# Optimization experiments

Hardware: AMD Instinct MI355X
Metric: run time of the kernel (lower is better)

Reference implementation:

```python
import jax, jax.numpy as jnp
import numpy as np
import math

EMBED_DIM = 1024
NUM_HEADS = 16
HEAD_DIM = EMBED_DIM // NUM_HEADS
MAX_POS = 512
SPARSE_TOPK = 32
B, T = 8, 512


def setup_inputs() -> dict:
    key = jax.random.key(0)
    ks = jax.random.split(key, 12)
    s = 1.0 / math.sqrt(EMBED_DIM)
    inp = {
        "x": jax.random.normal(ks[0], (B, T, EMBED_DIM), dtype=jnp.float32),
        "Wq": jax.random.uniform(ks[1], (EMBED_DIM, EMBED_DIM), jnp.float32, -s, s),
        "bq": jax.random.uniform(ks[2], (EMBED_DIM,), jnp.float32, -s, s),
        "Wk": jax.random.uniform(ks[3], (EMBED_DIM, EMBED_DIM), jnp.float32, -s, s),
        "bk": jax.random.uniform(ks[4], (EMBED_DIM,), jnp.float32, -s, s),
        "Wv": jax.random.uniform(ks[5], (EMBED_DIM, EMBED_DIM), jnp.float32, -s, s),
        "bv": jax.random.uniform(ks[6], (EMBED_DIM,), jnp.float32, -s, s),
        "Wo": jax.random.uniform(ks[7], (EMBED_DIM, EMBED_DIM), jnp.float32, -s, s),
        "bo": jax.random.uniform(ks[8], (EMBED_DIM,), jnp.float32, -s, s),
        "head_gates": jnp.ones((NUM_HEADS,), dtype=jnp.float32),
        "rel_bias": 0.02 * jax.random.normal(ks[9], (2 * MAX_POS - 1, NUM_HEADS), dtype=jnp.float32),
    }
    return inp


def reference(x, Wq, bq, Wk, bk, Wv, bv, Wo, bo, head_gates, rel_bias):
    Bb, Tt, C = x.shape
    H, D = NUM_HEADS, HEAD_DIM
    # projections -> [B, H, T, D]
    q = (x @ Wq.T + bq).reshape(Bb, Tt, H, D).transpose(0, 2, 1, 3)
    k = (x @ Wk.T + bk).reshape(Bb, Tt, H, D).transpose(0, 2, 1, 3)
    v = (x @ Wv.T + bv).reshape(Bb, Tt, H, D).transpose(0, 2, 1, 3)
    scores = jnp.einsum("bhqd,bhkd->bhqk", q, k) / math.sqrt(D)
    # gathered relative-position bias: rel[i,j] = j - i + MAX_POS - 1
    idx = jnp.arange(Tt)
    rel = idx[None, :] - idx[:, None] + (MAX_POS - 1)          # [T, T]
    pos_bias = rel_bias[rel].transpose(2, 0, 1)[None]          # [1, H, T, T]
    scores = scores + pos_bias
    if SPARSE_TOPK > 0:
        # keep only top-k entries per row; threshold == k-th largest value,
        # equivalent to torch.topk + scatter into a full -inf matrix
        topk_vals, _ = jax.lax.top_k(scores, SPARSE_TOPK)
        thresh = topk_vals[..., -1:]
        scores = jnp.where(scores >= thresh, scores, -jnp.inf)
    weights = jax.nn.softmax(scores, axis=-1)                  # dropout is identity (p=0, eval)
    gated = weights * head_gates[None, :, None, None]
    attn_out = jnp.einsum("bhqk,bhkd->bhqd", gated, v)
    attn_out = attn_out.transpose(0, 2, 1, 3).reshape(Bb, Tt, C)
    return attn_out @ Wo.T + bo
```

## Files before the change

### kernel.cpp

```cpp
#include <hip/hip_runtime.h>
#include <math.h>

#define EMBED 1024
#define NHEAD 16
#define HDIM  64
#define MAXPOS 512
#define TOPK  32
#define BB    8
#define TTT   512
#define BT    (BB*TTT)

__global__ __launch_bounds__(256, 2)
void gemm_qk_f64(const float* __restrict__ A,
                 const float* __restrict__ Wq, const float* __restrict__ bq_,
                 const float* __restrict__ Wk, const float* __restrict__ bk_,
                 float* __restrict__ outq, float* __restrict__ outk)
{
    __shared__ float As[16][132];
    __shared__ float Bs[16][68];
    const int t  = threadIdx.x;
    const int mb = blockIdx.x;
    const int yy = blockIdx.y;
    const int nb = yy & 15;
    const float* __restrict__ W    = (yy < 16) ? Wq  : Wk;
    const float* __restrict__ bias = (yy < 16) ? bq_ : bk_;
    float*                    out  = (yy < 16) ? outq : outk;
    const int tr = t >> 4, tc = t & 15;

    double acc[8][4] = {};

    for (int kt = 0; kt < 1024; kt += 16) {
        #pragma unroll
        for (int i = 0; i < 2; i++) {
            int L   = t + i * 256;
            int row = L >> 2;
            int cg  = (L & 3) * 4;
            float4 a4 = *(const float4*)&A[(size_t)(mb*128 + row)*1024 + kt + cg];
            As[cg+0][row] = a4.x; As[cg+1][row] = a4.y;
            As[cg+2][row] = a4.z; As[cg+3][row] = a4.w;
        }
        {
            int row = t >> 2, cg = (t & 3) * 4;
            float4 b4 = *(const float4*)&W[(size_t)(nb*64 + row)*1024 + kt + cg];
            Bs[cg+0][row] = b4.x; Bs[cg+1][row] = b4.y;
            Bs[cg+2][row] = b4.z; Bs[cg+3][row] = b4.w;
        }
        __syncthreads();
        #pragma unroll
        for (int kk = 0; kk < 16; kk++) {
            float a[8], bv[4];
            *(float4*)&a[0]  = *(const float4*)&As[kk][tr*8];
            *(float4*)&a[4]  = *(const float4*)&As[kk][tr*8+4];
            *(float4*)&bv[0] = *(const float4*)&Bs[kk][tc*4];
            double bd[4] = {(double)bv[0], (double)bv[1], (double)bv[2], (double)bv[3]};
            #pragma unroll
            for (int i = 0; i < 8; i++) {
                double ad = (double)a[i];
                #pragma unroll
                for (int j = 0; j < 4; j++)
                    acc[i][j] = fma(ad, bd[j], acc[i][j]);
            }
        }
        __syncthreads();
    }

    #pragma unroll
    for (int i = 0; i < 8; i++) {
        int token = mb*128 + tr*8 + i;
        int b  = token >> 9, tt = token & 511;
        int c0 = nb*64 + tc*4;
        float4 v;
        v.x = (float)(acc[i][0] + (double)bias[c0+0]);
        v.y = (float)(acc[i][1] + (double)bias[c0+1]);
        v.z = (float)(acc[i][2] + (double)bias[c0+2]);
        v.w = (float)(acc[i][3] + (double)bias[c0+3]);
        *(float4*)&out[(((size_t)b*NHEAD + nb)*TTT + tt)*HDIM + tc*4] = v;
    }
}

__global__ __launch_bounds__(256, 2)
void gemm_nt(const float* __restrict__ A, const float* __restrict__ W,
             const float* __restrict__ bias, float* __restrict__ out,
             int scatter)
{
    __shared__ float As[16][132];
    __shared__ float Bs[16][132];
    const int t  = threadIdx.x;
    const int mb = blockIdx.x;
    const int nb = blockIdx.y;
    const int tr = t >> 4, tc = t & 15;

    float acc[8][8] = {};

    for (int kt = 0; kt < 1024; kt += 16) {
        #pragma unroll
        for (int i = 0; i < 2; i++) {
            int L   = t + i * 256;
            int row = L >> 2;
            int cg  = (L & 3) * 4;
            float4 a4 = *(const float4*)&A[(size_t)(mb*128 + row)*1024 + kt + cg];
            As[cg+0][row] = a4.x; As[cg+1][row] = a4.y;
            As[cg+2][row] = a4.z; As[cg+3][row] = a4.w;
            float4 b4 = *(const float4*)&W[(size_t)(nb*128 + row)*1024 + kt + cg];
            Bs[cg+0][row] = b4.x; Bs[cg+1][row] = b4.y;
            Bs[cg+2][row] = b4.z; Bs[cg+3][row] = b4.w;
        }
        __syncthreads();
        #pragma unroll
        for (int kk = 0; kk < 16; kk++) {
            float a[8], bv[8];
            *(float4*)&a[0]  = *(const float4*)&As[kk][tr*8];
            *(float4*)&a[4]  = *(const float4*)&As[kk][tr*8+4];
            *(float4*)&bv[0] = *(const float4*)&Bs[kk][tc*8];
            *(float4*)&bv[4] = *(const float4*)&Bs[kk][tc*8+4];
            #pragma unroll
            for (int i = 0; i < 8; i++)
                #pragma unroll
                for (int j = 0; j < 8; j++)
                    acc[i][j] = fmaf(a[i], bv[j], acc[i][j]);
        }
        __syncthreads();
    }

    if (scatter) {
        #pragma unroll
        for (int i = 0; i < 8; i++) {
            int token = mb*128 + tr*8 + i;
            int b  = token >> 9, tt = token & 511;
            #pragma unroll
            for (int jg = 0; jg < 2; jg++) {
                int c = nb*128 + tc*8 + jg*4;
                int h = c >> 6, d = c & 63;
                float4 v;
                v.x = acc[i][jg*4+0] + bias[c+0];
                v.y = acc[i][jg*4+1] + bias[c+1];
                v.z = acc[i][jg*4+2] + bias[c+2];
                v.w = acc[i][jg*4+3] + bias[c+3];
                *(float4*)&out[(((size_t)b*NHEAD + h)*TTT + tt)*HDIM + d] = v;
            }
        }
    } else {
        #pragma unroll
        for (int i = 0; i < 8; i++) {
            int token = mb*128 + tr*8 + i;
            #pragma unroll
            for (int jg = 0; jg < 2; jg++) {
                int c = nb*128 + tc*8 + jg*4;
                float4 v;
                v.x = acc[i][jg*4+0] + bias[c+0];
                v.y = acc[i][jg*4+1] + bias[c+1];
                v.z = acc[i][jg*4+2] + bias[c+2];
                v.w = acc[i][jg*4+3] + bias[c+3];
                *(float4*)&out[(size_t)token*1024 + c] = v;
            }
        }
    }
}

__global__ __launch_bounds__(512, 4)
void attn_kernel(const float* __restrict__ qb, const float* __restrict__ kb,
                 const float* __restrict__ vb, const float* __restrict__ gates,
                 const float* __restrict__ relb, float* __restrict__ aout)
{
    __shared__ float qs[32][68];
    __shared__ union {
        float ks[128][68];
        struct { float w[32][64]; unsigned short c[32][64]; } sp;
    } u;

    const int t    = threadIdx.x;
    const int lane = t & 63, wv = t >> 6;
    const int qt   = blockIdx.x;
    const int bh   = blockIdx.y;
    const int h    = bh & 15, b = bh >> 4;
    const int qrow_g = qt * 32;
    const int r0   = wv * 4;

    const float* qbase = qb + ((size_t)bh*TTT + qrow_g)*HDIM;
    const float* kbase = kb + (size_t)bh*TTT*HDIM;
    const float* vbase = vb + (size_t)bh*TTT*HDIM;

    {
        int row = t >> 4, cg = (t & 15) * 4;
        *(float4*)&qs[row][cg] = *(const float4*)&qbase[(size_t)row*HDIM + cg];
    }

    float sc[4][8];

    #pragma unroll
    for (int ktile = 0; ktile < 4; ktile++) {
        __syncthreads();
        #pragma unroll
        for (int i = 0; i < 4; i++) {
            int L   = t + i * 512;
            int col = L >> 4, dg = (L & 15) * 4;
            *(float4*)&u.ks[col][dg] =
                *(const float4*)&kbase[(size_t)(ktile*128 + col)*HDIM + dg];
        }
        __syncthreads();

        double acc[4][2] = {};
        #pragma unroll 2
        for (int d = 0; d < 64; d += 4) {
            float4 k0 = *(const float4*)&u.ks[lane][d];
            float4 k1 = *(const float4*)&u.ks[lane+64][d];
            double k0d[4] = {(double)k0.x,(double)k0.y,(double)k0.z,(double)k0.w};
            double k1d[4] = {(double)k1.x,(double)k1.y,(double)k1.z,(double)k1.w};
            #pragma unroll
            for (int i = 0; i < 4; i++) {
                float4 q4 = *(const float4*)&qs[r0+i][d];
                double q0 = (double)q4.x, q1 = (double)q4.y;
                double q2 = (double)q4.z, q3 = (double)q4.w;
                acc[i][0] = fma(q0, k0d[0], acc[i][0]);
                acc[i][0] = fma(q1, k0d[1], acc[i][0]);
                acc[i][0] = fma(q2, k0d[2], acc[i][0]);
                acc[i][0] = fma(q3, k0d[3], acc[i][0]);
                acc[i][1] = fma(q0, k1d[0], acc[i][1]);
                acc[i][1] = fma(q1, k1d[1], acc[i][1]);
                acc[i][1] = fma(q2, k1d[2], acc[i][1]);
                acc[i][1] = fma(q3, k1d[3], acc[i][1]);
            }
        }
        #pragma unroll
        for (int i = 0; i < 4; i++) {
            int rg = qrow_g + r0 + i;
            #pragma unroll
            for (int s01 = 0; s01 < 2; s01++) {
                int c = ktile*128 + lane + 64*s01;
                sc[i][2*ktile+s01] = (float)(acc[i][s01]*0.125 +
                                     (double)relb[(size_t)(c - rg + 511)*NHEAD + h]);
            }
        }
    }
    __syncthreads();

    float val[4][8];
    #pragma unroll
    for (int i = 0; i < 4; i++)
        #pragma unroll
        for (int j = 0; j < 8; j++) val[i][j] = sc[i][j];

    float rowmax[4], thresh[4];
    #pragma unroll 1
    for (int it = 0; it < TOPK; it++) {
        #pragma unroll
        for (int rr = 0; rr < 4; rr++) {
            float lm = val[rr][0];
            #pragma unroll
            for (int j = 1; j < 8; j++) lm = fmaxf(lm, val[rr][j]);
            float m = lm;
            #pragma unroll
            for (int off = 32; off >= 1; off >>= 1)
                m = fmaxf(m, __shfl_xor(m, off));
            if (it == 0) rowmax[rr] = m;
            thresh[rr] = m;
            unsigned long long ball = __ballot(lm == m);
            int first = __ffsll(ball) - 1;
            if (lane == first) {
                bool done = false;
                #pragma unroll
                for (int j = 0; j < 8; j++)
                    if (!done && val[rr][j] == m) { val[rr][j] = -__builtin_inff(); done = true; }
            }
        }
    }

    const float gate = gates[h];
    #pragma unroll
    for (int rr = 0; rr < 4; rr++) {
        int row = r0 + rr;
        float w[8];
        float sum = 0.f;
        #pragma unroll
        for (int j = 0; j < 8; j++) {
            float sv = sc[rr][j];
            float wv2 = (sv >= thresh[rr]) ? __expf(sv - rowmax[rr]) : 0.f;
            w[j] = wv2;
            sum += wv2;
        }
        #pragma unroll
        for (int off = 32; off >= 1; off >>= 1)
            sum += __shfl_xor(sum, off);
        float rscale = gate / sum;

        int n = 0;
        #pragma unroll
        for (int j = 0; j < 8; j++) {
            bool keep = (sc[rr][j] >= thresh[rr]);
            unsigned long long mask = __ballot(keep);
            int pos = n + __popcll(mask & ((1ull << lane) - 1ull));
            if (keep && pos < 64) {
                u.sp.c[row][pos] = (unsigned short)(lane + 64*j);
                u.sp.w[row][pos] = w[j];
            }
            n += __popcll(mask);
        }
        if (n > 64) n = 64;

        float o = 0.f;
        int e = 0;
        for (; e + 4 <= n; e += 4) {
            int   c0 = u.sp.c[row][e],   c1 = u.sp.c[row][e+1];
            int   c2 = u.sp.c[row][e+2], c3 = u.sp.c[row][e+3];
            float w0 = u.sp.w[row][e],   w1 = u.sp.w[row][e+1];
            float w2 = u.sp.w[row][e+2], w3 = u.sp.w[row][e+3];
            float v0 = vbase[(size_t)c0*HDIM + lane];
            float v1 = vbase[(size_t)c1*HDIM + lane];
            float v2 = vbase[(size_t)c2*HDIM + lane];
            float v3 = vbase[(size_t)c3*HDIM + lane];
            o = fmaf(w0, v0, o);
            o = fmaf(w1, v1, o);
            o = fmaf(w2, v2, o);
            o = fmaf(w3, v3, o);
        }
        for (; e < n; e++) {
            int   c = u.sp.c[row][e];
            float wv2 = u.sp.w[row][e];
            o = fmaf(wv2, vbase[(size_t)c*HDIM + lane], o);
        }

        aout[((size_t)(b*TTT + qrow_g + row))*EMBED + h*HDIM + lane] = o * rscale;
    }
}

extern "C" void kernel_launch(void* const* d_in, const int* in_sizes, int n_in,
                              void* d_out, int out_size, void* d_ws, size_t ws_size,
                              hipStream_t stream) {
    const float* x     = (const float*)d_in[0];
    const float* Wq    = (const float*)d_in[1];
    const float* bq    = (const float*)d_in[2];
    const float* Wk    = (const float*)d_in[3];
    const float* bk    = (const float*)d_in[4];
    const float* Wv    = (const float*)d_in[5];
    const float* bv    = (const float*)d_in[6];
    const float* Wo    = (const float*)d_in[7];
    const float* bo    = (const float*)d_in[8];
    const float* gates = (const float*)d_in[9];
    const float* relb  = (const float*)d_in[10];
    float* out = (float*)d_out;

    const size_t SZ = (size_t)BT * EMBED;
    float* qb = (float*)d_ws;
    float* kb = qb + SZ;
    float* vb = kb + SZ;
    float* ab = vb + SZ;

    gemm_qk_f64<<<dim3(32,32), dim3(256), 0, stream>>>(x, Wq, bq, Wk, bk, qb, kb);
    gemm_nt<<<dim3(32,8), dim3(256), 0, stream>>>(x, Wv, bv, vb, 1);
    attn_kernel<<<dim3(16,128), dim3(512), 0, stream>>>(qb, kb, vb, gates, relb, ab);
    gemm_nt<<<dim3(32,8), dim3(256), 0, stream>>>(ab, Wo, bo, out, 0);
}
```

Measured before the change: 1.199 ms.

## Compute attention scores in fp32 with fp64 recompute only near top-k threshold

Switches the QK^T score accumulation in the attention kernel from double to float. A row is recomputed in double precision from global K, and its top-k threshold reselected, only when at least two scores fall within a small epsilon of the threshold. This avoids slow fp64 FMA throughput on the common path while trying to keep top-k selection consistent with the reference at near-ties. Occupancy hint is lowered from 4 to 2 and the per-row loop is no longer unrolled, which may cost latency hiding.

```diff
diff --git a/kernel.cpp b/kernel.cpp
--- a/kernel.cpp
+++ b/kernel.cpp
@@ -9,6 +9,7 @@
 #define BB    8
 #define TTT   512
 #define BT    (BB*TTT)
+#define SCORE_EPS 1e-4f
 
 __global__ __launch_bounds__(256, 2)
 void gemm_qk_f64(const float* __restrict__ A,
@@ -157,7 +158,7 @@
     }
 }
 
-__global__ __launch_bounds__(512, 4)
+__global__ __launch_bounds__(512, 2)
 void attn_kernel(const float* __restrict__ qb, const float* __restrict__ kb,
                  const float* __restrict__ vb, const float* __restrict__ gates,
                  const float* __restrict__ relb, float* __restrict__ aout)
@@ -199,26 +200,22 @@
         }
         __syncthreads();
 
-        double acc[4][2] = {};
-        #pragma unroll 2
+        float acc[4][2] = {};
+        #pragma unroll 4
         for (int d = 0; d < 64; d += 4) {
             float4 k0 = *(const float4*)&u.ks[lane][d];
             float4 k1 = *(const float4*)&u.ks[lane+64][d];
-            double k0d[4] = {(double)k0.x,(double)k0.y,(double)k0.z,(double)k0.w};
-            double k1d[4] = {(double)k1.x,(double)k1.y,(double)k1.z,(double)k1.w};
             #pragma unroll
             for (int i = 0; i < 4; i++) {
                 float4 q4 = *(const float4*)&qs[r0+i][d];
-                double q0 = (double)q4.x, q1 = (double)q4.y;
-                double q2 = (double)q4.z, q3 = (double)q4.w;
-                acc[i][0] = fma(q0, k0d[0], acc[i][0]);
-                acc[i][0] = fma(q1, k0d[1], acc[i][0]);
-                acc[i][0] = fma(q2, k0d[2], acc[i][0]);
-                acc[i][0] = fma(q3, k0d[3], acc[i][0]);
-                acc[i][1] = fma(q0, k1d[0], acc[i][1]);
-                acc[i][1] = fma(q1, k1d[1], acc[i][1]);
-                acc[i][1] = fma(q2, k1d[2], acc[i][1]);
-                acc[i][1] = fma(q3, k1d[3], acc[i][1]);
+                acc[i][0] = fmaf(q4.x, k0.x, acc[i][0]);
+                acc[i][0] = fmaf(q4.y, k0.y, acc[i][0]);
+                acc[i][0] = fmaf(q4.z, k0.z, acc[i][0]);
+                acc[i][0] = fmaf(q4.w, k0.w, acc[i][0]);
+                acc[i][1] = fmaf(q4.x, k1.x, acc[i][1]);
+                acc[i][1] = fmaf(q4.y, k1.y, acc[i][1]);
+                acc[i][1] = fmaf(q4.z, k1.z, acc[i][1]);
+                acc[i][1] = fmaf(q4.w, k1.w, acc[i][1]);
             }
         }
         #pragma unroll
@@ -227,8 +224,8 @@
             #pragma unroll
             for (int s01 = 0; s01 < 2; s01++) {
                 int c = ktile*128 + lane + 64*s01;
-                sc[i][2*ktile+s01] = (float)(acc[i][s01]*0.125 +
-                                     (double)relb[(size_t)(c - rg + 511)*NHEAD + h]);
+                sc[i][2*ktile+s01] = acc[i][s01]*0.125f +
+                                     relb[(size_t)(c - rg + 511)*NHEAD + h];
             }
         }
     }
@@ -266,9 +263,60 @@
     }
 
     const float gate = gates[h];
-    #pragma unroll
+    #pragma unroll 1
     for (int rr = 0; rr < 4; rr++) {
         int row = r0 + rr;
+
+        int band = 0;
+        #pragma unroll
+        for (int j = 0; j < 8; j++) {
+            bool inb = fabsf(sc[rr][j] - thresh[rr]) <= SCORE_EPS;
+            band += __popcll(__ballot(inb));
+        }
+        if (band >= 2) {
+            int rg = qrow_g + row;
+            #pragma unroll 1
+            for (int j = 0; j < 8; j++) {
+                int c = lane + 64*j;
+                const float* kc = kbase + (size_t)c*HDIM;
+                double a = 0.0;
+                #pragma unroll 4
+                for (int d = 0; d < 64; d += 4) {
+                    float4 kv = *(const float4*)&kc[d];
+                    float4 q4 = *(const float4*)&qs[row][d];
+                    a = fma((double)q4.x, (double)kv.x, a);
+                    a = fma((double)q4.y, (double)kv.y, a);
+                    a = fma((double)q4.z, (double)kv.z, a);
+                    a = fma((double)q4.w, (double)kv.w, a);
+                }
+                sc[rr][j] = (float)(a*0.125 +
+                            (double)relb[(size_t)(c - rg + 511)*NHEAD + h]);
+            }
+            float v2[8];
+            #pragma unroll
+            for (int j = 0; j < 8; j++) v2[j] = sc[rr][j];
+            #pragma unroll 1
+            for (int it = 0; it < TOPK; it++) {
+                float lm = v2[0];
+                #pragma unroll
+                for (int j = 1; j < 8; j++) lm = fmaxf(lm, v2[j]);
+                float m = lm;
+                #pragma unroll
+                for (int off = 32; off >= 1; off >>= 1)
+                    m = fmaxf(m, __shfl_xor(m, off));
+                if (it == 0) rowmax[rr] = m;
+                thresh[rr] = m;
+                unsigned long long ball = __ballot(lm == m);
+                int first = __ffsll(ball) - 1;
+                if (lane == first) {
+                    bool done = false;
+                    #pragma unroll
+                    for (int j = 0; j < 8; j++)
+                        if (!done && v2[j] == m) { v2[j] = -__builtin_inff(); done = true; }
+                }
+            }
+        }
+
         float w[8];
         float sum = 0.f;
         #pragma unroll
@@ -306,11 +354,11 @@
             float w2 = u.sp.w[row][e+2], w3 = u.sp.w[row][e+3];
             float v0 = vbase[(size_t)c0*HDIM + lane];
             float v1 = vbase[(size_t)c1*HDIM + lane];
-            float v2 = vbase[(size_t)c2*HDIM + lane];
+            float v2_ = vbase[(size_t)c2*HDIM + lane];
             float v3 = vbase[(size_t)c3*HDIM + lane];
             o = fmaf(w0, v0, o);
             o = fmaf(w1, v1, o);
-            o = fmaf(w2, v2, o);
+            o = fmaf(w2, v2_, o);
             o = fmaf(w3, v3, o);
         }
         for (; e < n; e++) {
```

Result: slower. 1.666 ms (+38.9%).
